# Kernel tuning notes

Measured on AMD Instinct MI355X. Metric: run time of the kernel, lower is better.

Reference implementation:

```python
import jax, jax.numpy as jnp
import numpy as np

NUM_EXPERTS = 8
HIDDEN = 2048
EXPERT_DIM = 4096
R = 64
LORA_ALPHA = 16
SCALING = LORA_ALPHA / R
TOKENS_PER_EXPERT = 1024


def setup_inputs() -> dict:
    key = jax.random.key(0)
    ks = jax.random.split(key, 7)
    s = lambda shape: 1.0 / np.sqrt(shape[-1])
    return {
        "hidden_states": jax.random.normal(ks[0], (NUM_EXPERTS * TOKENS_PER_EXPERT, HIDDEN), jnp.float32),
        "W_gu": jax.random.normal(ks[1], (2 * EXPERT_DIM, HIDDEN), jnp.float32) * s((HIDDEN,)),
        "A_gu": jax.random.normal(ks[2], (R, HIDDEN), jnp.float32) * s((HIDDEN,)),
        "B_gu": jax.random.normal(ks[3], (2 * EXPERT_DIM, R), jnp.float32) * 0.01,
        "W_d": jax.random.normal(ks[4], (HIDDEN, EXPERT_DIM), jnp.float32) * s((EXPERT_DIM,)),
        "A_d": jax.random.normal(ks[5], (R, EXPERT_DIM), jnp.float32) * s((EXPERT_DIM,)),
        "B_d": jax.random.normal(ks[6], (HIDDEN, R), jnp.float32) * 0.01,
    }


def _lora_linear(x, W, A, B):
    # y = x @ W^T + scaling * (x @ A^T) @ B^T   (nn.Linear convention, no dropout)
    return x @ W.T + (x @ A.T) @ B.T * SCALING


def reference(hidden_states, W_gu, A_gu, B_gu, W_d, A_d, B_d):
    # (E, N, H)
    x = hidden_states.reshape(NUM_EXPERTS, -1, HIDDEN)
    gate_up = _lora_linear(x, W_gu, A_gu, B_gu)          # (E, N, 2*D)
    gate, up = jnp.split(gate_up, 2, axis=-1)             # each (E, N, D)
    h = up * jax.nn.silu(gate)                            # SwiGLU
    out = _lora_linear(h, W_d, A_d, B_d)                  # (E, N, H)
    return out.reshape(-1, HIDDEN)
```

## Files before the change

### kernel.cpp

```cpp
#include <hip/hip_runtime.h>
#include <stdint.h>

typedef __bf16 bf16_t;
typedef __bf16 bf16x8 __attribute__((ext_vector_type(8)));
typedef __bf16 bf16x4 __attribute__((ext_vector_type(4)));
typedef float f32x4 __attribute__((ext_vector_type(4)));

#define GLOAD16(gp, lp)                                                        \
    __builtin_amdgcn_global_load_lds(                                          \
        (const __attribute__((address_space(1))) void*)(gp),                   \
        (__attribute__((address_space(3))) void*)(lp), 16, 0, 0)

#define MFMA16(a, b, c) __builtin_amdgcn_mfma_f32_16x16x32_bf16(a, b, c, 0, 0, 0)

#define PH_PRE()                                                               \
    do {                                                                       \
        __builtin_amdgcn_sched_barrier(0);                                     \
        asm volatile("s_barrier" ::: "memory");                                \
        asm volatile("s_waitcnt lgkmcnt(0)" ::: "memory");                     \
        __builtin_amdgcn_sched_barrier(0);                                     \
        __builtin_amdgcn_s_setprio(1);                                         \
    } while (0)
#define PH_POST()                                                              \
    do {                                                                       \
        __builtin_amdgcn_s_setprio(0);                                         \
        __builtin_amdgcn_sched_barrier(0);                                     \
        asm volatile("s_barrier" ::: "memory");                                \
    } while (0)


__global__ __launch_bounds__(256) void cvt_all_kernel(
    const float* __restrict__ x, const float* __restrict__ Wgu,
    const float* __restrict__ Bgu, const float* __restrict__ Wd,
    const float* __restrict__ Bd, const float* __restrict__ Agu,
    const float* __restrict__ Ad, bf16_t* __restrict__ X1,
    bf16_t* __restrict__ W1, bf16_t* __restrict__ W2,
    bf16_t* __restrict__ Abf, bf16_t* __restrict__ Adbf) {
    int b = blockIdx.x;
    const float* src;
    bf16_t* dst;
    int cshift, cmask, ldd, coff, lb;
    if (b < 16384) {
        src = x; dst = X1; cshift = 11; cmask = 2047; ldd = 2112; coff = 0; lb = b;
    } else if (b < 32768) {
        src = Wgu; dst = W1; cshift = 11; cmask = 2047; ldd = 2112; coff = 0; lb = b - 16384;
    } else if (b < 33280) {
        src = Bgu; dst = W1; cshift = 6; cmask = 63; ldd = 2112; coff = 2048; lb = b - 32768;
    } else if (b < 41472) {
        src = Wd; dst = W2; cshift = 12; cmask = 4095; ldd = 4160; coff = 0; lb = b - 33280;
    } else if (b < 41600) {
        src = Bd; dst = W2; cshift = 6; cmask = 63; ldd = 4160; coff = 4096; lb = b - 41472;
    } else if (b < 41728) {
        src = Agu; dst = Abf; cshift = 11; cmask = 2047; ldd = 2048; coff = 0; lb = b - 41600;
    } else {
        src = Ad; dst = Adbf; cshift = 12; cmask = 4095; ldd = 4096; coff = 0; lb = b - 41728;
    }
    int idx = (lb * 256 + threadIdx.x) << 2;
    int r = idx >> cshift;
    int c = idx & cmask;
    float4 v = *(const float4*)(src + idx);
    bf16x4 o = {(bf16_t)v.x, (bf16_t)v.y, (bf16_t)v.z, (bf16_t)v.w};
    *(bf16x4*)(dst + (size_t)r * ldd + coff + c) = o;
}

__global__ __launch_bounds__(256) void lora_kernel(const bf16_t* __restrict__ A,
                                                   int lda,
                                                   const bf16_t* __restrict__ Bw,
                                                   int K, bf16_t* __restrict__ dst,
                                                   int ldd, int coff) {
    __shared__ __align__(16) bf16_t As[64 * 64];
    __shared__ __align__(16) bf16_t Bs[64 * 64];
    const int t = threadIdx.x;
    const int m0 = blockIdx.x * 64;
    const int lane = t & 63, w = t >> 6;
    const int ln15 = lane & 15, q = lane >> 4;

    const int lrow = t >> 3;
    const int lchunk = (t & 7) ^ (lrow & 7);
    const bf16_t* gaL = A + (size_t)(m0 + lrow) * lda + lchunk * 8;
    const bf16_t* gbL = Bw + (size_t)lrow * K + lchunk * 8;
    bf16_t* lA = As + t * 8;
    bf16_t* lB = Bs + t * 8;

    const f32x4 z = {0.f, 0.f, 0.f, 0.f};
    f32x4 acc[4];
#pragma unroll
    for (int j = 0; j < 4; ++j) acc[j] = z;

    int aoffs[2], boffs[2][4];
#pragma unroll
    for (int s = 0; s < 2; ++s) {
        int rowa = w * 16 + ln15;
        aoffs[s] = rowa * 64 + (((q + 4 * s) ^ (rowa & 7)) << 3);
#pragma unroll
        for (int j = 0; j < 4; ++j) {
            int rowb = j * 16 + ln15;
            boffs[s][j] = rowb * 64 + (((q + 4 * s) ^ (rowb & 7)) << 3);
        }
    }

    for (int kt = 0; kt < K; kt += 64) {
        GLOAD16(gaL, lA);
        GLOAD16(gaL + (size_t)32 * lda, lA + 32 * 64);
        GLOAD16(gbL, lB);
        GLOAD16(gbL + (size_t)32 * K, lB + 32 * 64);
        __syncthreads();
#pragma unroll
        for (int s = 0; s < 2; ++s) {
            bf16x8 av = *(const bf16x8*)(As + aoffs[s]);
#pragma unroll
            for (int j = 0; j < 4; ++j) {
                bf16x8 bv = *(const bf16x8*)(Bs + boffs[s][j]);
                acc[j] = MFMA16(av, bv, acc[j]);
            }
        }
        __syncthreads();
        gaL += 64;
        gbL += 64;
    }

#pragma unroll
    for (int j = 0; j < 4; ++j)
#pragma unroll
        for (int rg = 0; rg < 4; ++rg) {
            int m = m0 + w * 16 + q * 4 + rg;
            dst[(size_t)m * ldd + coff + j * 16 + ln15] = (bf16_t)(acc[j][rg] * 0.25f);
        }
}

template <int LDA_, int LDB_, int NT_>
__device__ __forceinline__ void gemm8p_core(const bf16_t* __restrict__ gA,
                                            const bf16_t* __restrict__ gB0,
                                            const bf16_t* __restrict__ gB2,
                                            bf16_t* smem, const int t,
                                            const int offA0, const int offA1,
                                            const int offB0, const int offB1,
                                            f32x4 (&acc)[8][4]) {
    auto stgA0 = [&](int kt, bf16_t* d) {
        GLOAD16(gA + kt, d + t * 8);
        GLOAD16(gA + (size_t)128 * LDA_ + kt, d + 128 * 64 + t * 8);
    };
    auto stgA1 = [&](int kt, bf16_t* d) {
        GLOAD16(gA + (size_t)64 * LDA_ + kt, d + 64 * 64 + t * 8);
        GLOAD16(gA + (size_t)192 * LDA_ + kt, d + 192 * 64 + t * 8);
    };
    auto stgBlo = [&](int kt, bf16_t* d) {
        GLOAD16(gB0 + kt, d + t * 8);
        GLOAD16(gB0 + (size_t)64 * LDB_ + kt, d + 64 * 64 + t * 8);
    };
    auto stgBhi = [&](int kt, bf16_t* d) {
        GLOAD16(gB2 + kt, d + 128 * 64 + t * 8);
        GLOAD16(gB2 + (size_t)64 * LDB_ + kt, d + 192 * 64 + t * 8);
    };

    bf16_t* const As0 = smem;
    bf16_t* const As1 = smem + 16384;
    bf16_t* const Bs0 = smem + 32768;
    bf16_t* const Bs1 = smem + 49152;

    stgA0(0, As0);
    stgA1(0, As0);
    stgBlo(0, Bs0);
    stgBhi(0, Bs0);
    stgA0(64, As1);
    stgBlo(64, Bs1);
    stgBhi(64, Bs1);
    asm volatile("s_waitcnt vmcnt(6)" ::: "memory");
    asm volatile("s_barrier" ::: "memory");

    bf16x8 av[4][2], b0[2][2], b1[2][2];
    for (int g = 0; g < NT_; ++g) {
        const int bs = (g & 1) << 14;
        bf16_t* const Asc = smem + bs;
        bf16_t* const Bsc = smem + 32768 + bs;
        bf16_t* const Asn = smem + (bs ^ 16384);
        const int k1 = (g + 1) << 6, k2 = (g + 2) << 6;

#pragma unroll
        for (int m = 0; m < 4; ++m) {
            av[m][0] = *(const bf16x8*)(Asc + offA0 + m * 1024);
            av[m][1] = *(const bf16x8*)(Asc + offA1 + m * 1024);
        }
#pragma unroll
        for (int n = 0; n < 2; ++n) {
            b0[n][0] = *(const bf16x8*)(Bsc + offB0 + n * 1024);
            b0[n][1] = *(const bf16x8*)(Bsc + offB1 + n * 1024);
        }
        if (g + 1 < NT_) stgA1(k1, Asn);
        PH_PRE();
#pragma unroll
        for (int m = 0; m < 4; ++m)
#pragma unroll
            for (int n = 0; n < 2; ++n) {
                acc[m][n] = MFMA16(av[m][0], b0[n][0], acc[m][n]);
                acc[m][n] = MFMA16(av[m][1], b0[n][1], acc[m][n]);
            }
        PH_POST();

#pragma unroll
        for (int n = 0; n < 2; ++n) {
            b1[n][0] = *(const bf16x8*)(Bsc + offB0 + (2 + n) * 1024);
            b1[n][1] = *(const bf16x8*)(Bsc + offB1 + (2 + n) * 1024);
        }
        if (g + 2 < NT_) stgA0(k2, Asc);
        PH_PRE();
#pragma unroll
        for (int m = 0; m < 4; ++m)
#pragma unroll
            for (int n = 0; n < 2; ++n) {
                acc[m][2 + n] = MFMA16(av[m][0], b1[n][0], acc[m][2 + n]);
                acc[m][2 + n] = MFMA16(av[m][1], b1[n][1], acc[m][2 + n]);
            }
        PH_POST();

#pragma unroll
        for (int m = 0; m < 4; ++m) {
            av[m][0] = *(const bf16x8*)(Asc + offA0 + (4 + m) * 1024);
            av[m][1] = *(const bf16x8*)(Asc + offA1 + (4 + m) * 1024);
        }
        if (g + 2 < NT_) stgBlo(k2, Bsc);
        PH_PRE();
#pragma unroll
        for (int m = 0; m < 4; ++m)
#pragma unroll
            for (int n = 0; n < 2; ++n) {
                acc[4 + m][2 + n] = MFMA16(av[m][0], b1[n][0], acc[4 + m][2 + n]);
                acc[4 + m][2 + n] = MFMA16(av[m][1], b1[n][1], acc[4 + m][2 + n]);
            }
        PH_POST();

        if (g + 2 < NT_) stgBhi(k2, Bsc);
        PH_PRE();
#pragma unroll
        for (int m = 0; m < 4; ++m)
#pragma unroll
            for (int n = 0; n < 2; ++n) {
                acc[4 + m][n] = MFMA16(av[m][0], b0[n][0], acc[4 + m][n]);
                acc[4 + m][n] = MFMA16(av[m][1], b0[n][1], acc[4 + m][n]);
            }
        __builtin_amdgcn_s_setprio(0);
        __builtin_amdgcn_sched_barrier(0);
        if (g + 2 < NT_)
            asm volatile("s_waitcnt vmcnt(6)" ::: "memory");
        else
            asm volatile("s_waitcnt vmcnt(0)" ::: "memory");
        asm volatile("s_barrier" ::: "memory");
    }
}

__global__ __launch_bounds__(512, 2) void gemm1_8p_kernel(
    const bf16_t* __restrict__ X, const bf16_t* __restrict__ Wc,
    bf16_t* __restrict__ X2) {
    __shared__ __align__(16) bf16_t smem[65536];
    const int t = threadIdx.x;
    const int lane = t & 63, wid = t >> 6;
    const int wr = wid >> 2, wc = wid & 3;
    const int ln15 = lane & 15, q = lane >> 4;
    const int n0 = blockIdx.x * 128;
    const int m0 = blockIdx.y * 256;

    const int sw = ln15 & 7;
    const int offA0 = (wr * 128 + ln15) * 64 + ((q ^ sw) << 3);
    const int offA1 = (wr * 128 + ln15) * 64 + (((q + 4) ^ sw) << 3);
    const int offB0 = (wc * 64 + ln15) * 64 + ((q ^ sw) << 3);
    const int offB1 = (wc * 64 + ln15) * 64 + (((q + 4) ^ sw) << 3);

    const int rr = t >> 3;
    const int lch = (t & 7) ^ (rr & 7);
    const bf16_t* gA = X + (size_t)(m0 + rr) * 2112 + lch * 8;
    const bf16_t* gB0 = Wc + (size_t)(n0 + rr) * 2112 + lch * 8;
    const bf16_t* gB2 = Wc + (size_t)(4096 + n0 + rr) * 2112 + lch * 8;

    f32x4 acc[8][4];
    const f32x4 z = {0.f, 0.f, 0.f, 0.f};
#pragma unroll
    for (int i = 0; i < 8; ++i)
#pragma unroll
        for (int j = 0; j < 4; ++j) acc[i][j] = z;

    gemm8p_core<2112, 2112, 33>(gA, gB0, gB2, smem, t, offA0, offA1, offB0,
                                offB1, acc);

    __syncthreads();
    float* fs = (float*)smem;
    if (wc >= 2) {
#pragma unroll
        for (int mi = 0; mi < 8; ++mi)
#pragma unroll
            for (int nj = 0; nj < 4; ++nj)
#pragma unroll
                for (int rg = 0; rg < 4; ++rg) {
                    int row = wr * 128 + mi * 16 + q * 4 + rg;
                    int col = (wc - 2) * 64 + nj * 16 + ln15;
                    fs[row * 128 + col] = acc[mi][nj][rg];
                }
    }
    __syncthreads();
    if (wc < 2) {
#pragma unroll
        for (int mi = 0; mi < 8; ++mi)
#pragma unroll
            for (int nj = 0; nj < 4; ++nj)
#pragma unroll
                for (int rg = 0; rg < 4; ++rg) {
                    int row = wr * 128 + mi * 16 + q * 4 + rg;
                    int col = wc * 64 + nj * 16 + ln15;
                    float gv = acc[mi][nj][rg];
                    float uv = fs[row * 128 + col];
                    float h = uv * gv / (1.f + __expf(-gv));
                    X2[(size_t)(m0 + row) * 4160 + (n0 + col)] = (bf16_t)h;
                }
    }
}

__global__ __launch_bounds__(512, 2) void gemm2_8p_kernel(
    const bf16_t* __restrict__ X2, const bf16_t* __restrict__ Wdc,
    float* __restrict__ out) {
    __shared__ __align__(16) bf16_t smem[65536];
    const int t = threadIdx.x;
    const int lane = t & 63, wid = t >> 6;
    const int wr = wid >> 2, wc = wid & 3;
    const int ln15 = lane & 15, q = lane >> 4;
    const int n0 = blockIdx.x * 256;
    const int m0 = blockIdx.y * 256;

    const int sw = ln15 & 7;
    const int offA0 = (wr * 128 + ln15) * 64 + ((q ^ sw) << 3);
    const int offA1 = (wr * 128 + ln15) * 64 + (((q + 4) ^ sw) << 3);
    const int offB0 = (wc * 64 + ln15) * 64 + ((q ^ sw) << 3);
    const int offB1 = (wc * 64 + ln15) * 64 + (((q + 4) ^ sw) << 3);

    const int rr = t >> 3;
    const int lch = (t & 7) ^ (rr & 7);
    const bf16_t* gA = X2 + (size_t)(m0 + rr) * 4160 + lch * 8;
    const bf16_t* gB0 = Wdc + (size_t)(n0 + rr) * 4160 + lch * 8;
    const bf16_t* gB2 = Wdc + (size_t)(n0 + 128 + rr) * 4160 + lch * 8;

    f32x4 acc[8][4];
    const f32x4 z = {0.f, 0.f, 0.f, 0.f};
#pragma unroll
    for (int i = 0; i < 8; ++i)
#pragma unroll
        for (int j = 0; j < 4; ++j) acc[i][j] = z;

    gemm8p_core<4160, 4160, 65>(gA, gB0, gB2, smem, t, offA0, offA1, offB0,
                                offB1, acc);

#pragma unroll
    for (int mi = 0; mi < 8; ++mi)
#pragma unroll
        for (int nj = 0; nj < 4; ++nj)
#pragma unroll
            for (int rg = 0; rg < 4; ++rg) {
                int row = wr * 128 + mi * 16 + q * 4 + rg;
                int col = wc * 64 + nj * 16 + ln15;
                out[(size_t)(m0 + row) * 2048 + (n0 + col)] = acc[mi][nj][rg];
            }
}

extern "C" void kernel_launch(void* const* d_in, const int* in_sizes, int n_in,
                              void* d_out, int out_size, void* d_ws, size_t ws_size,
                              hipStream_t stream) {
    const float* x = (const float*)d_in[0];
    const float* Wgu = (const float*)d_in[1];
    const float* Agu = (const float*)d_in[2];
    const float* Bgu = (const float*)d_in[3];
    const float* Wd = (const float*)d_in[4];
    const float* Ad = (const float*)d_in[5];
    const float* Bd = (const float*)d_in[6];
    float* out = (float*)d_out;

    char* ws = (char*)d_ws;
    bf16_t* X1 = (bf16_t*)(ws);
    bf16_t* W1 = (bf16_t*)(ws + 34603008);
    bf16_t* X2 = (bf16_t*)(ws + 69206016);
    bf16_t* W2 = (bf16_t*)(ws + 137363456);
    bf16_t* Abf = (bf16_t*)(ws + 154402816);
    bf16_t* Adbf = (bf16_t*)(ws + 154664960);

    cvt_all_kernel<<<41984, 256, 0, stream>>>(x, Wgu, Bgu, Wd, Bd, Agu, Ad,
                                              X1, W1, W2, Abf, Adbf);

    lora_kernel<<<128, 256, 0, stream>>>(X1, 2112, Abf, 2048, X1, 2112, 2048);
    gemm1_8p_kernel<<<dim3(32, 32), 512, 0, stream>>>(X1, W1, X2);
    lora_kernel<<<128, 256, 0, stream>>>(X2, 4160, Adbf, 4096, X2, 4160, 4096);
    gemm2_8p_kernel<<<dim3(8, 32), 512, 0, stream>>>(X2, W2, out);
}
```

Measured before the change: 627.8 us.

## Software-pipeline LDS fragment loads across MFMA phases and swizzle epilogue scratch

```diff
diff --git a/kernel.cpp b/kernel.cpp
--- a/kernel.cpp
+++ b/kernel.cpp
@@ -13,19 +13,53 @@
 
 #define MFMA16(a, b, c) __builtin_amdgcn_mfma_f32_16x16x32_bf16(a, b, c, 0, 0, 0)
 
-#define PH_PRE()                                                               \
+#define SB() __builtin_amdgcn_sched_barrier(0)
+#define BAR() asm volatile("s_barrier" ::: "memory")
+#define LGKM0() asm volatile("s_waitcnt lgkmcnt(0)" ::: "memory")
+#define VMW(n) asm volatile("s_waitcnt vmcnt(" #n ")" ::: "memory")
+
+#define PHASE(GATE, STAGE, PF, MM)                                             \
     do {                                                                       \
-        __builtin_amdgcn_sched_barrier(0);                                     \
-        asm volatile("s_barrier" ::: "memory");                                \
-        asm volatile("s_waitcnt lgkmcnt(0)" ::: "memory");                     \
-        __builtin_amdgcn_sched_barrier(0);                                     \
+        GATE;                                                                  \
+        STAGE;                                                                 \
+        SB();                                                                  \
+        BAR();                                                                 \
+        LGKM0();                                                               \
+        SB();                                                                  \
         __builtin_amdgcn_s_setprio(1);                                         \
+        PF;                                                                    \
+        SB();                                                                  \
+        MM;                                                                    \
+        __builtin_amdgcn_s_setprio(0);                                         \
+        SB();                                                                  \
+        BAR();                                                                 \
     } while (0)
-#define PH_POST()                                                              \
+
+#define MMCL(aa, bb, mo, no)                                                   \
     do {                                                                       \
-        __builtin_amdgcn_s_setprio(0);                                         \
-        __builtin_amdgcn_sched_barrier(0);                                     \
-        asm volatile("s_barrier" ::: "memory");                                \
+        _Pragma("unroll") for (int m_ = 0; m_ < 4; ++m_) {                     \
+            _Pragma("unroll") for (int n_ = 0; n_ < 2; ++n_) {                 \
+                acc[mo + m_][no + n_] =                                        \
+                    MFMA16(aa[m_][0], bb[n_][0], acc[mo + m_][no + n_]);       \
+                acc[mo + m_][no + n_] =                                        \
+                    MFMA16(aa[m_][1], bb[n_][1], acc[mo + m_][no + n_]);       \
+            }                                                                  \
+        }                                                                      \
+    } while (0)
+
+#define PFA(dst, base, ro)                                                     \
+    do {                                                                       \
+        _Pragma("unroll") for (int m_ = 0; m_ < 4; ++m_) {                     \
+            dst[m_][0] = *(const bf16x8*)((base) + offA0 + (ro + m_) * 1024);  \
+            dst[m_][1] = *(const bf16x8*)((base) + offA1 + (ro + m_) * 1024);  \
+        }                                                                      \
+    } while (0)
+#define PFB(dst, base, no)                                                     \
+    do {                                                                       \
+        _Pragma("unroll") for (int n_ = 0; n_ < 2; ++n_) {                     \
+            dst[n_][0] = *(const bf16x8*)((base) + offB0 + (no + n_) * 1024);  \
+            dst[n_][1] = *(const bf16x8*)((base) + offB1 + (no + n_) * 1024);  \
+        }                                                                      \
     } while (0)
 
 
@@ -136,6 +170,12 @@
                                             const int offA0, const int offA1,
                                             const int offB0, const int offB1,
                                             f32x4 (&acc)[8][4]) {
+    static_assert(NT_ & 1, "NT_ must be odd (pairs + tail tile)");
+    bf16_t* const As0 = smem;
+    bf16_t* const As1 = smem + 16384;
+    bf16_t* const Bs0 = smem + 32768;
+    bf16_t* const Bs1 = smem + 49152;
+
     auto stgA0 = [&](int kt, bf16_t* d) {
         GLOAD16(gA + kt, d + t * 8);
         GLOAD16(gA + (size_t)128 * LDA_ + kt, d + 128 * 64 + t * 8);
@@ -153,10 +193,7 @@
         GLOAD16(gB2 + (size_t)64 * LDB_ + kt, d + 192 * 64 + t * 8);
     };
 
-    bf16_t* const As0 = smem;
-    bf16_t* const As1 = smem + 16384;
-    bf16_t* const Bs0 = smem + 32768;
-    bf16_t* const Bs1 = smem + 49152;
+    bf16x8 a0[4][2], a1[4][2], b0e[2][2], b0o[2][2], b1v[2][2];
 
     stgA0(0, As0);
     stgA1(0, As0);
@@ -165,87 +202,36 @@
     stgA0(64, As1);
     stgBlo(64, Bs1);
     stgBhi(64, Bs1);
-    asm volatile("s_waitcnt vmcnt(6)" ::: "memory");
-    asm volatile("s_barrier" ::: "memory");
-
-    bf16x8 av[4][2], b0[2][2], b1[2][2];
-    for (int g = 0; g < NT_; ++g) {
-        const int bs = (g & 1) << 14;
-        bf16_t* const Asc = smem + bs;
-        bf16_t* const Bsc = smem + 32768 + bs;
-        bf16_t* const Asn = smem + (bs ^ 16384);
-        const int k1 = (g + 1) << 6, k2 = (g + 2) << 6;
-
-#pragma unroll
-        for (int m = 0; m < 4; ++m) {
-            av[m][0] = *(const bf16x8*)(Asc + offA0 + m * 1024);
-            av[m][1] = *(const bf16x8*)(Asc + offA1 + m * 1024);
-        }
-#pragma unroll
-        for (int n = 0; n < 2; ++n) {
-            b0[n][0] = *(const bf16x8*)(Bsc + offB0 + n * 1024);
-            b0[n][1] = *(const bf16x8*)(Bsc + offB1 + n * 1024);
-        }
-        if (g + 1 < NT_) stgA1(k1, Asn);
-        PH_PRE();
-#pragma unroll
-        for (int m = 0; m < 4; ++m)
-#pragma unroll
-            for (int n = 0; n < 2; ++n) {
-                acc[m][n] = MFMA16(av[m][0], b0[n][0], acc[m][n]);
-                acc[m][n] = MFMA16(av[m][1], b0[n][1], acc[m][n]);
-            }
-        PH_POST();
-
-#pragma unroll
-        for (int n = 0; n < 2; ++n) {
-            b1[n][0] = *(const bf16x8*)(Bsc + offB0 + (2 + n) * 1024);
-            b1[n][1] = *(const bf16x8*)(Bsc + offB1 + (2 + n) * 1024);
-        }
-        if (g + 2 < NT_) stgA0(k2, Asc);
-        PH_PRE();
-#pragma unroll
-        for (int m = 0; m < 4; ++m)
-#pragma unroll
-            for (int n = 0; n < 2; ++n) {
-                acc[m][2 + n] = MFMA16(av[m][0], b1[n][0], acc[m][2 + n]);
-                acc[m][2 + n] = MFMA16(av[m][1], b1[n][1], acc[m][2 + n]);
-            }
-        PH_POST();
-
-#pragma unroll
-        for (int m = 0; m < 4; ++m) {
-            av[m][0] = *(const bf16x8*)(Asc + offA0 + (4 + m) * 1024);
-            av[m][1] = *(const bf16x8*)(Asc + offA1 + (4 + m) * 1024);
-        }
-        if (g + 2 < NT_) stgBlo(k2, Bsc);
-        PH_PRE();
-#pragma unroll
-        for (int m = 0; m < 4; ++m)
-#pragma unroll
-            for (int n = 0; n < 2; ++n) {
-                acc[4 + m][2 + n] = MFMA16(av[m][0], b1[n][0], acc[4 + m][2 + n]);
-                acc[4 + m][2 + n] = MFMA16(av[m][1], b1[n][1], acc[4 + m][2 + n]);
-            }
-        PH_POST();
-
-        if (g + 2 < NT_) stgBhi(k2, Bsc);
-        PH_PRE();
-#pragma unroll
-        for (int m = 0; m < 4; ++m)
-#pragma unroll
-            for (int n = 0; n < 2; ++n) {
-                acc[4 + m][n] = MFMA16(av[m][0], b0[n][0], acc[4 + m][n]);
-                acc[4 + m][n] = MFMA16(av[m][1], b0[n][1], acc[4 + m][n]);
-            }
-        __builtin_amdgcn_s_setprio(0);
-        __builtin_amdgcn_sched_barrier(0);
-        if (g + 2 < NT_)
-            asm volatile("s_waitcnt vmcnt(6)" ::: "memory");
-        else
-            asm volatile("s_waitcnt vmcnt(0)" ::: "memory");
-        asm volatile("s_barrier" ::: "memory");
-    }
+    VMW(6);
+    BAR();
+    PFA(a0, As0, 0);
+    PFB(b0e, Bs0, 0);
+
+    for (int g = 0; g + 2 < NT_; g += 2) {
+        const int k1 = (g + 1) << 6, k2 = (g + 2) << 6, k3 = (g + 3) << 6;
+        const bool s3 = (g + 3 < NT_);
+
+        PHASE((void)0, stgA1(k1, As1), PFB(b1v, Bs0, 2), MMCL(a0, b0e, 0, 0));
+        PHASE((void)0, stgA0(k2, As0), PFA(a1, As0, 4), MMCL(a0, b1v, 0, 2));
+        PHASE(VMW(4), stgBlo(k2, Bs0), PFB(b0o, Bs1, 0), MMCL(a1, b1v, 4, 2));
+        PHASE((void)0, stgBhi(k2, Bs0), PFA(a0, As1, 0), MMCL(a1, b0e, 4, 0));
+        PHASE((void)0, stgA1(k2, As0), PFB(b1v, Bs1, 2), MMCL(a0, b0o, 0, 0));
+        PHASE(VMW(8), if (s3) stgA0(k3, As1), PFA(a1, As1, 4),
+              MMCL(a0, b1v, 0, 2));
+        PHASE(VMW(2), if (s3) stgBlo(k3, Bs1), PFB(b0e, Bs0, 0),
+              MMCL(a1, b1v, 4, 2));
+        PHASE((void)0, if (s3) stgBhi(k3, Bs1), PFA(a0, As0, 0),
+              MMCL(a1, b0o, 4, 0));
+    }
+
+    PHASE((void)0, (void)0, PFB(b1v, Bs0, 2), MMCL(a0, b0e, 0, 0));
+    PHASE(VMW(0), (void)0, PFA(a1, As0, 4), MMCL(a0, b1v, 0, 2));
+    PHASE((void)0, (void)0, (void)0, MMCL(a1, b1v, 4, 2));
+    PHASE((void)0, (void)0, (void)0, MMCL(a1, b0e, 4, 0));
+}
+
+__device__ __forceinline__ int eswz(int row, int col) {
+    return col ^ (((row >> 2) & 1) << 4) ^ (((row >> 3) & 3) << 2);
 }
 
 __global__ __launch_bounds__(512, 2) void gemm1_8p_kernel(
@@ -292,7 +278,7 @@
                 for (int rg = 0; rg < 4; ++rg) {
                     int row = wr * 128 + mi * 16 + q * 4 + rg;
                     int col = (wc - 2) * 64 + nj * 16 + ln15;
-                    fs[row * 128 + col] = acc[mi][nj][rg];
+                    fs[row * 128 + eswz(row, col)] = acc[mi][nj][rg];
                 }
     }
     __syncthreads();
@@ -306,7 +292,7 @@
                     int row = wr * 128 + mi * 16 + q * 4 + rg;
                     int col = wc * 64 + nj * 16 + ln15;
                     float gv = acc[mi][nj][rg];
-                    float uv = fs[row * 128 + col];
+                    float uv = fs[row * 128 + eswz(row, col)];
                     float h = uv * gv / (1.f + __expf(-gv));
                     X2[(size_t)(m0 + row) * 4160 + (n0 + col)] = (bf16_t)h;
                 }
```

New measurement: 662.8 us. +5.6%, slower.
